# Optimization experiments

Hardware: AMD Instinct MI355X
Metric: run time of the kernel (lower is better)

The kernel has to match this reference:

```python
import jax, jax.numpy as jnp
import numpy as np

EPS = 1e-4

def setup_inputs() -> dict:
    key = jax.random.key(0)
    k1, k2, k3 = jax.random.split(key, 3)
    batch, keysize, dict_size, categories = 4096, 512, 16384, 100
    x = jax.random.normal(k1, (batch, keysize), dtype=jnp.float32)
    keys = jax.random.normal(k2, (dict_size, keysize), dtype=jnp.float32) * 0.1  # TruncatedNormal(0, 0.1) approx
    values = jax.random.uniform(k3, (dict_size, categories), dtype=jnp.float32)
    return {"x": x, "keys": keys, "values": values}


def reference(x, keys, values):
    # sq_distance(keys, x): (dict_size, batch)
    kk = jnp.sum(keys * keys, axis=1)[:, None]          # (D, 1)
    xx = jnp.sum(x * x, axis=1)[None, :]                # (1, B)
    d = kk - 2.0 * jnp.matmul(keys, x.T) + xx           # (D, B)
    kern = 1.0 / (d + EPS)                              # reciprocal kernel
    # transpose -> (B, D), matmul values (D, C) -> (B, C)
    return jnp.matmul(kern.T, values)
```

## Files before the change

### kernel.cpp

```cpp
#include <hip/hip_runtime.h>
#include <hip/hip_bf16.h>
#include <hip/hip_fp8.h>
#include <cstdint>


#define BSZ   4096
#define DSZ   16384
#define KSZ   512
#define CC    100
#define CP    128
#define EPSV  1e-4f

#define BM     64
#define BD     64
#define DSPLIT 8
#define DCHUNK (DSZ / DSPLIT)
#define NITER  (DCHUNK / BD)
#define KTS    72

typedef short  short8 __attribute__((ext_vector_type(8)));
typedef float  f32x4  __attribute__((ext_vector_type(4)));
typedef long   lng2   __attribute__((ext_vector_type(2)));
typedef unsigned int   u32;
typedef unsigned short u16;
typedef unsigned char  u8;

__device__ __forceinline__ u16 f2bf(float f) {
    union { float f; u32 u; } cv; cv.f = f;
    u32 u = cv.u;
    u += 0x7fffu + ((u >> 16) & 1u);
    return (u16)(u >> 16);
}
__device__ __forceinline__ u32 pack2(float a, float b) {
    return (u32)f2bf(a) | ((u32)f2bf(b) << 16);
}
__device__ __forceinline__ u8 f2fp8(float f) {
    __hip_fp8_e4m3 t(f);
    return *reinterpret_cast<u8*>(&t);
}

__device__ __forceinline__ void gload_lds16(const void* g, void* l) {
    __builtin_amdgcn_global_load_lds(
        (const __attribute__((address_space(1))) u32*)g,
        (__attribute__((address_space(3))) u32*)l, 16, 0, 0);
}


__global__ __launch_bounds__(256)
void convert_xk(const float* __restrict__ x, const float* __restrict__ keys,
                u8* __restrict__ xw, u8* __restrict__ kw,
                float* __restrict__ kk, float* __restrict__ xx)
{
    const int tid = threadIdx.x, wid = tid >> 6, lane = tid & 63;
    const int row = blockIdx.x * 4 + wid;
    const float* src; u8* dst; float* nrm; int r;
    if (row < DSZ) { r = row;       src = keys + (size_t)r * KSZ; dst = kw + (size_t)r * KSZ; nrm = kk + r; }
    else           { r = row - DSZ; src = x    + (size_t)r * KSZ; dst = xw + (size_t)r * KSZ; nrm = xx + r; }

    float4 v0 = *reinterpret_cast<const float4*>(src + lane * 8);
    float4 v1 = *reinterpret_cast<const float4*>(src + lane * 8 + 4);
    float s = v0.x*v0.x + v0.y*v0.y + v0.z*v0.z + v0.w*v0.w
            + v1.x*v1.x + v1.y*v1.y + v1.z*v1.z + v1.w*v1.w;

    unsigned long long pk = 0;
    pk |= (unsigned long long)f2fp8(v0.x);
    pk |= (unsigned long long)f2fp8(v0.y) << 8;
    pk |= (unsigned long long)f2fp8(v0.z) << 16;
    pk |= (unsigned long long)f2fp8(v0.w) << 24;
    pk |= (unsigned long long)f2fp8(v1.x) << 32;
    pk |= (unsigned long long)f2fp8(v1.y) << 40;
    pk |= (unsigned long long)f2fp8(v1.z) << 48;
    pk |= (unsigned long long)f2fp8(v1.w) << 56;

    const int j = lane >> 2, hi_l = lane & 3;
    const int ch = j >> 3, jl = j & 7, jj = jl >> 1, f = jl & 1;
    const int off = ch * 256 + (((jj * 64 + hi_l * 16)) ^ ((r & 7) << 4)) + f * 8;
    *reinterpret_cast<unsigned long long*>(dst + off) = pk;

    s += __shfl_xor(s, 1);  s += __shfl_xor(s, 2);  s += __shfl_xor(s, 4);
    s += __shfl_xor(s, 8);  s += __shfl_xor(s, 16); s += __shfl_xor(s, 32);
    if (lane == 0) *nrm = s;
}

__global__ __launch_bounds__(256)
void convert_v(const float* __restrict__ values, u16* __restrict__ vw)
{
    const int gid = blockIdx.x * 256 + threadIdx.x;
    const int c = gid >> 11;
    const int j = gid & 2047;
    const int dp  = ((j >> 3) << 6) + ((j & 7) << 3);
    const int dsg = ((j >> 3) << 6) + (((j & 7) ^ (c & 7)) << 3);
    uint4 w = make_uint4(0, 0, 0, 0);
    if (c < CC) {
        float f[8];
#pragma unroll
        for (int i = 0; i < 8; ++i) f[i] = values[(size_t)(dsg + i) * CC + c];
        w.x = pack2(f[0], f[1]); w.y = pack2(f[2], f[3]);
        w.z = pack2(f[4], f[5]); w.w = pack2(f[6], f[7]);
    }
    *reinterpret_cast<uint4*>(vw + (size_t)c * DSZ + dp) = w;
}

__global__ __launch_bounds__(512, 4)
void varkeys_fast(const u8* __restrict__ xw, const u8* __restrict__ kw,
                  const u16* __restrict__ vw, const float* __restrict__ kkp,
                  const float* __restrict__ xxp, float* __restrict__ out)
{
    __shared__ __align__(16) u8  ksb0[BD * 256];
    __shared__ __align__(16) u8  ksb1[BD * 256];
    __shared__ __align__(16) u16 kT[BM * KTS];
    __shared__ __align__(16) u16 vT[CP * BD];
    __shared__ float xx_s[BM];

    const int tid  = threadIdx.x;
    const int wid  = tid >> 6;
    const int lane = tid & 63;
    const int lo   = lane & 15;
    const int hi   = lane >> 4;
    const int wm   = wid >> 1;
    const int wn   = wid & 1;

    const int h  = blockIdx.x;
    const int by = h & 7, bx = h >> 3;
    const int bm0   = bx * BM;
    const int dbase = by * DCHUNK;

    if (tid < BM) xx_s[tid] = xxp[bm0 + tid];

    lng2 xq[8];
    {
        const int row = bm0 + wm * 16 + lo;
        const u8* base = xw + (size_t)row * KSZ;
        const int s16 = (row & 7) << 4;
#pragma unroll
        for (int ch = 0; ch < 2; ++ch)
#pragma unroll
            for (int jj = 0; jj < 4; ++jj)
                xq[ch * 4 + jj] = *reinterpret_cast<const lng2*>(
                    base + ch * 256 + ((jj * 64 + hi * 16) ^ s16));
    }

    f32x4 accO[4];
#pragma unroll
    for (int n = 0; n < 4; ++n) accO[n] = f32x4{0.f, 0.f, 0.f, 0.f};

#define IS_KS(BUFP, DK, CCH) { \
        _Pragma("unroll") \
        for (int i = 0; i < 2; ++i) { \
            const int ci = wid * 2 + i; \
            const int flat = ci * 1024 + lane * 16; \
            gload_lds16(kw + (size_t)((DK) + (flat >> 8)) * KSZ + (CCH) * 256 + (flat & 255), \
                        (char*)(BUFP) + ci * 1024); \
        } }

#define IS_VT(D0) { \
        _Pragma("unroll") \
        for (int i = 0; i < 2; ++i) { \
            const int ci = wid * 2 + i; \
            const int flat = ci * 512 + lane * 8; \
            gload_lds16(vw + (size_t)(flat >> 6) * DSZ + (D0) + (flat & 63), \
                        (char*)vT + ci * 1024); \
        } }

    IS_KS(ksb0, dbase, 0)
    asm volatile("s_waitcnt lgkmcnt(0)" ::: "memory");
    __builtin_amdgcn_s_barrier();

    const int swz   = (lo & 7) << 3;
    const int swz16 = (lo & 7) << 4;

#define A16(CH, BUF)                                                                  \
    {                                                                                 \
        _Pragma("unroll")                                                             \
        for (int jj = 0; jj < 4; ++jj) {                                              \
            const int off = (jj * 64 + hi * 16) ^ swz16;                              \
            const u8* p0 = (const u8*)(BUF) + (wn * 32 + lo) * 256 + off;             \
            lng2 b0 = *reinterpret_cast<const lng2*>(p0);                             \
            lng2 b1 = *reinterpret_cast<const lng2*>(p0 + 16 * 256);                  \
            lng2 a0 = xq[(CH) * 4 + jj];                                              \
            accS[0] = __builtin_amdgcn_mfma_f32_16x16x32_fp8_fp8(a0[0], b0[0], accS[0], 0, 0, 0); \
            accS[1] = __builtin_amdgcn_mfma_f32_16x16x32_fp8_fp8(a0[0], b1[0], accS[1], 0, 0, 0); \
            accS[0] = __builtin_amdgcn_mfma_f32_16x16x32_fp8_fp8(a0[1], b0[1], accS[0], 0, 0, 0); \
            accS[1] = __builtin_amdgcn_mfma_f32_16x16x32_fp8_fp8(a0[1], b1[1], accS[1], 0, 0, 0); \
        }                                                                             \
    }

    for (int it = 0; it < NITER; ++it) {
        const int d0 = dbase + it * BD;

        f32x4 accS[2];
#pragma unroll
        for (int n = 0; n < 2; ++n) accS[n] = f32x4{0.f, 0.f, 0.f, 0.f};

        __builtin_amdgcn_s_barrier();
        IS_KS(ksb1, d0, 1)
        IS_VT(d0)
        const float kkf0 = kkp[d0 + wn * 32 + lo];
        const float kkf1 = kkp[d0 + wn * 32 + 16 + lo];
        asm volatile("s_waitcnt vmcnt(6)" ::: "memory");
        __builtin_amdgcn_s_barrier();
        __builtin_amdgcn_sched_barrier(0);
        A16(0, ksb0)

        __builtin_amdgcn_s_barrier();
        if (it < NITER - 1) {
            IS_KS(ksb0, d0 + BD, 0)
            asm volatile("s_waitcnt vmcnt(6)" ::: "memory");
        } else {
            asm volatile("s_waitcnt vmcnt(0)" ::: "memory");
        }
        __builtin_amdgcn_s_barrier();
        __builtin_amdgcn_sched_barrier(0);
        A16(1, ksb1)

#pragma unroll
        for (int n = 0; n < 2; ++n) {
            const int dl = wn * 32 + n * 16 + lo;
            const float kkv = n ? kkf1 : kkf0;
#pragma unroll
            for (int r = 0; r < 4; ++r) {
                const int rowl = wm * 16 + hi * 4 + r;
                const float dsq = kkv + xx_s[rowl] - 2.f * accS[n][r] + EPSV;
                kT[rowl * KTS + dl] = f2bf(__builtin_amdgcn_rcpf(dsq));
            }
        }
        asm volatile("s_waitcnt vmcnt(2)" ::: "memory");
        asm volatile("s_waitcnt lgkmcnt(0)" ::: "memory");
        __builtin_amdgcn_s_barrier();
        __builtin_amdgcn_sched_barrier(0);

#pragma unroll
        for (int kst = 0; kst < 2; ++kst) {
            const int k0l = kst * 32 + hi * 8;
            const int k0v = k0l ^ swz;
            short8 a0 = *reinterpret_cast<const short8*>(&kT[(wm * 16 + lo) * KTS + k0l]);
#pragma unroll
            for (int nh = 0; nh < 2; ++nh) {
                short8 b0 = *reinterpret_cast<const short8*>(&vT[(wn * 64 + nh * 32 + lo) * BD + k0v]);
                short8 b1 = *reinterpret_cast<const short8*>(&vT[(wn * 64 + nh * 32 + 16 + lo) * BD + k0v]);
                accO[nh * 2 + 0] = __builtin_amdgcn_mfma_f32_16x16x32_bf16(a0, b0, accO[nh * 2 + 0], 0, 0, 0);
                accO[nh * 2 + 1] = __builtin_amdgcn_mfma_f32_16x16x32_bf16(a0, b1, accO[nh * 2 + 1], 0, 0, 0);
            }
        }
    }

#pragma unroll
    for (int n = 0; n < 4; ++n) {
        const int c = wn * 64 + n * 16 + lo;
        if (c < CC) {
#pragma unroll
            for (int r = 0; r < 4; ++r) {
                const int b_ = bm0 + wm * 16 + hi * 4 + r;
                atomicAdd(&out[(size_t)b_ * CC + c], accO[n][r]);
            }
        }
    }
#undef IS_KS
#undef IS_VT
#undef A16
}


#define FBM 128
#define XS_STRIDE 72
#define KS_STRIDE 72
#define KT_STRIDE 72
#define VL_STRIDE 106
#define FKC 64
#define FNKC (KSZ / FKC)
#define FDSPLIT 8
#define FDCHUNK (DSZ / FDSPLIT)
#define FNITER  (FDCHUNK / BD)

__global__ __launch_bounds__(256)
void varkeys_pre(const float* __restrict__ x, const float* __restrict__ keys,
                 float* __restrict__ kk, float* __restrict__ xx)
{
    const int tid  = threadIdx.x;
    const int wid  = tid >> 6;
    const int lane = tid & 63;
    const int lo   = lane & 15;
    const int sub  = lane >> 4;
    const int row  = blockIdx.x * 16 + wid * 4 + sub;
    const float* src = (row < DSZ) ? keys + (size_t)row * KSZ
                                   : x + (size_t)(row - DSZ) * KSZ;
    float s = 0.f;
#pragma unroll
    for (int j = 0; j < 8; ++j) {
        float4 v = *reinterpret_cast<const float4*>(src + j * 64 + lo * 4);
        s += v.x * v.x + v.y * v.y + v.z * v.z + v.w * v.w;
    }
    s += __shfl_xor(s, 1); s += __shfl_xor(s, 2);
    s += __shfl_xor(s, 4); s += __shfl_xor(s, 8);
    if (lo == 0) {
        if (row < DSZ) kk[row] = s;
        else           xx[row - DSZ] = s;
    }
}

__global__ __launch_bounds__(256, 2)
void varkeys_main(const float* __restrict__ x, const float* __restrict__ keys,
                  const float* __restrict__ values, float* __restrict__ out,
                  const float* __restrict__ kk_ws, const float* __restrict__ xx_ws,
                  int use_ws)
{
    __shared__ __align__(16) u16 xs[FBM * XS_STRIDE];
    __shared__ __align__(16) u16 ks[BD * KS_STRIDE];
    __shared__ __align__(16) u16 kTf[FBM * KT_STRIDE];
    __shared__ __align__(16) u16 vls[BD * VL_STRIDE];
    __shared__ float kk_s[FDCHUNK];
    __shared__ float xx_s[FBM];

    const int tid  = threadIdx.x;
    const int wid  = tid >> 6;
    const int lane = tid & 63;
    const int lo   = lane & 15;
    const int hi   = lane >> 4;
    const int wm   = wid >> 1;
    const int wn   = wid & 1;
    const int bm0   = blockIdx.x * FBM;
    const int dbase = blockIdx.y * FDCHUNK;

    if (use_ws) {
        for (int i = tid; i < FDCHUNK; i += 256) kk_s[i] = kk_ws[dbase + i];
        if (tid < FBM) xx_s[tid] = xx_ws[bm0 + tid];
    } else {
        for (int rbase = wid * 4; rbase < FDCHUNK + FBM; rbase += 16) {
            const int row = rbase + hi;
            const float* src = (row < FDCHUNK)
                ? keys + (size_t)(dbase + row) * KSZ
                : x + (size_t)(bm0 + row - FDCHUNK) * KSZ;
            float s = 0.f;
#pragma unroll
            for (int j = 0; j < 8; ++j) {
                float4 v = *reinterpret_cast<const float4*>(src + j * 64 + lo * 4);
                s += v.x * v.x + v.y * v.y + v.z * v.z + v.w * v.w;
            }
            s += __shfl_xor(s, 1); s += __shfl_xor(s, 2);
            s += __shfl_xor(s, 4); s += __shfl_xor(s, 8);
            if (lo == 0) {
                if (row < FDCHUNK) kk_s[row] = s;
                else               xx_s[row - FDCHUNK] = s;
            }
        }
    }
    __syncthreads();

    f32x4 accO[4][4];
#pragma unroll
    for (int m = 0; m < 4; ++m)
#pragma unroll
        for (int n = 0; n < 4; ++n) accO[m][n] = f32x4{0.f, 0.f, 0.f, 0.f};

    for (int it = 0; it < FNITER; ++it) {
        const int d0 = dbase + it * BD;

        f32x4 accS[4][2];
#pragma unroll
        for (int m = 0; m < 4; ++m)
#pragma unroll
            for (int n = 0; n < 2; ++n) accS[m][n] = f32x4{0.f, 0.f, 0.f, 0.f};

        for (int kc = 0; kc < FNKC; ++kc) {
            __syncthreads();
#pragma unroll
            for (int j = 0; j < 8; ++j) {
                const int idx = tid + j * 256;
                const int row = idx >> 4, c4 = idx & 15;
                float4 v = *reinterpret_cast<const float4*>(
                    x + (size_t)(bm0 + row) * KSZ + kc * FKC + c4 * 4);
                u32* dst = reinterpret_cast<u32*>(&xs[row * XS_STRIDE + c4 * 4]);
                dst[0] = pack2(v.x, v.y); dst[1] = pack2(v.z, v.w);
            }
#pragma unroll
            for (int j = 0; j < 4; ++j) {
                const int idx = tid + j * 256;
                const int row = idx >> 4, c4 = idx & 15;
                float4 v = *reinterpret_cast<const float4*>(
                    keys + (size_t)(d0 + row) * KSZ + kc * FKC + c4 * 4);
                u32* dst = reinterpret_cast<u32*>(&ks[row * KS_STRIDE + c4 * 4]);
                dst[0] = pack2(v.x, v.y); dst[1] = pack2(v.z, v.w);
            }
            __syncthreads();
#pragma unroll
            for (int kst = 0; kst < 2; ++kst) {
                const int k0 = kst * 32 + hi * 8;
                short8 a[4], b[2];
#pragma unroll
                for (int m = 0; m < 4; ++m)
                    a[m] = *reinterpret_cast<const short8*>(
                        &xs[(wm * 64 + m * 16 + lo) * XS_STRIDE + k0]);
#pragma unroll
                for (int n = 0; n < 2; ++n)
                    b[n] = *reinterpret_cast<const short8*>(
                        &ks[(wn * 32 + n * 16 + lo) * KS_STRIDE + k0]);
#pragma unroll
                for (int m = 0; m < 4; ++m)
#pragma unroll
                    for (int n = 0; n < 2; ++n)
                        accS[m][n] = __builtin_amdgcn_mfma_f32_16x16x32_bf16(
                            a[m], b[n], accS[m][n], 0, 0, 0);
            }
        }

#pragma unroll
        for (int m = 0; m < 4; ++m)
#pragma unroll
            for (int n = 0; n < 2; ++n) {
                const int dl = wn * 32 + n * 16 + lo;
                const float kkv = kk_s[it * BD + dl];
#pragma unroll
                for (int r = 0; r < 4; ++r) {
                    const int bl = wm * 64 + m * 16 + hi * 4 + r;
                    const float dsq = kkv + xx_s[bl] - 2.f * accS[m][n][r] + EPSV;
                    kTf[bl * KT_STRIDE + dl] = f2bf(__builtin_amdgcn_rcpf(dsq));
                }
            }

#pragma unroll
        for (int j = 0; j < 7; ++j) {
            const int idx = tid + j * 256;
            if (idx < 1600) {
                const int row = idx / 25, c4 = idx % 25;
                float4 v = *reinterpret_cast<const float4*>(
                    values + (size_t)(d0 + row) * CC + c4 * 4);
                u32* dst = reinterpret_cast<u32*>(&vls[row * VL_STRIDE + c4 * 4]);
                dst[0] = pack2(v.x, v.y); dst[1] = pack2(v.z, v.w);
            }
        }
        __syncthreads();

#pragma unroll
        for (int ks2 = 0; ks2 < 2; ++ks2) {
            const int k0 = ks2 * 32 + hi * 8;
            short8 a[4], b[4];
#pragma unroll
            for (int m = 0; m < 4; ++m)
                a[m] = *reinterpret_cast<const short8*>(
                    &kTf[(wm * 64 + m * 16 + lo) * KT_STRIDE + k0]);
#pragma unroll
            for (int n = 0; n < 4; ++n) {
                const int c = wn * 64 + n * 16 + lo;
                short8 t = {0, 0, 0, 0, 0, 0, 0, 0};
                if (c < CC) {
#pragma unroll
                    for (int i = 0; i < 8; ++i)
                        t[i] = (short)vls[(k0 + i) * VL_STRIDE + c];
                }
                b[n] = t;
            }
#pragma unroll
            for (int m = 0; m < 4; ++m)
#pragma unroll
                for (int n = 0; n < 4; ++n)
                    accO[m][n] = __builtin_amdgcn_mfma_f32_16x16x32_bf16(
                        a[m], b[n], accO[m][n], 0, 0, 0);
        }
    }

#pragma unroll
    for (int m = 0; m < 4; ++m)
#pragma unroll
        for (int n = 0; n < 4; ++n) {
            const int c = wn * 64 + n * 16 + lo;
            if (c < CC) {
#pragma unroll
                for (int r = 0; r < 4; ++r) {
                    const int b_ = bm0 + wm * 64 + m * 16 + hi * 4 + r;
                    atomicAdd(&out[(size_t)b_ * CC + c], accO[m][n][r]);
                }
            }
        }
}

extern "C" void kernel_launch(void* const* d_in, const int* in_sizes, int n_in,
                              void* d_out, int out_size, void* d_ws, size_t ws_size,
                              hipStream_t stream) {
    const float* x      = (const float*)d_in[0];
    const float* keys   = (const float*)d_in[1];
    const float* values = (const float*)d_in[2];
    float* out = (float*)d_out;

    hipMemsetAsync(d_out, 0, (size_t)out_size * sizeof(float), stream);

    const size_t off_xw = 0;
    const size_t off_kw = off_xw + (size_t)BSZ * KSZ;
    const size_t off_vw = off_kw + (size_t)DSZ * KSZ;
    const size_t off_kk = off_vw + (size_t)CP * DSZ * 2;
    const size_t off_xx = off_kk + (size_t)DSZ * 4;
    const size_t need   = off_xx + (size_t)BSZ * 4;

    if (ws_size >= need) {
        u8*  xw = (u8*)((char*)d_ws + off_xw);
        u8*  kw = (u8*)((char*)d_ws + off_kw);
        u16* vw = (u16*)((char*)d_ws + off_vw);
        float* kk = (float*)((char*)d_ws + off_kk);
        float* xx = (float*)((char*)d_ws + off_xx);
        convert_xk<<<dim3((DSZ + BSZ) / 4), dim3(256), 0, stream>>>(x, keys, xw, kw, kk, xx);
        convert_v<<<dim3((CP * DSZ / 8) / 256), dim3(256), 0, stream>>>(values, vw);
        varkeys_fast<<<dim3(DSPLIT * (BSZ / BM)), dim3(512), 0, stream>>>(xw, kw, vw, kk, xx, out);
    } else {
        const size_t ws_need = (size_t)(DSZ + BSZ) * sizeof(float);
        const int use_ws = (ws_size >= ws_need) ? 1 : 0;
        float* kk = (float*)d_ws;
        float* xx = kk + DSZ;
        if (use_ws) {
            varkeys_pre<<<dim3((DSZ + BSZ) / 16), dim3(256), 0, stream>>>(x, keys, kk, xx);
        }
        varkeys_main<<<dim3(BSZ / FBM, FDSPLIT), dim3(256), 0, stream>>>(
            x, keys, values, out, kk, xx, use_ws);
    }
}
```

Baseline: 114.6 us.

## Merge conversion kernels, keep x norms in registers, skip padded-column MFMAs

The two preprocessing kernels become one launch whose blocks branch by index into either the x/keys fp8 conversion or the values bf16 transpose, removing one launch and its gap. The main kernel drops the shared xx buffer and loads each row's norm, with epsilon folded in, straight into registers. It also removes the initial lgkmcnt wait. It skips the last 16-column MFMA and its LDS load for the second wave column, since those columns are padding beyond 100 categories. The savings are small per-iteration costs, and the register norm load adds a few global loads per thread.

```diff
diff --git a/kernel.cpp b/kernel.cpp
--- a/kernel.cpp
+++ b/kernel.cpp
@@ -45,60 +45,62 @@
         (__attribute__((address_space(3))) u32*)l, 16, 0, 0);
 }
 
+#define XK_BLOCKS ((DSZ + BSZ) / 4)
+#define V_BLOCKS  ((CP * DSZ / 8) / 256)
 
 __global__ __launch_bounds__(256)
-void convert_xk(const float* __restrict__ x, const float* __restrict__ keys,
-                u8* __restrict__ xw, u8* __restrict__ kw,
-                float* __restrict__ kk, float* __restrict__ xx)
+void convert_all(const float* __restrict__ x, const float* __restrict__ keys,
+                 const float* __restrict__ values,
+                 u8* __restrict__ xw, u8* __restrict__ kw, u16* __restrict__ vw,
+                 float* __restrict__ kk, float* __restrict__ xx)
 {
-    const int tid = threadIdx.x, wid = tid >> 6, lane = tid & 63;
-    const int row = blockIdx.x * 4 + wid;
-    const float* src; u8* dst; float* nrm; int r;
-    if (row < DSZ) { r = row;       src = keys + (size_t)r * KSZ; dst = kw + (size_t)r * KSZ; nrm = kk + r; }
-    else           { r = row - DSZ; src = x    + (size_t)r * KSZ; dst = xw + (size_t)r * KSZ; nrm = xx + r; }
-
-    float4 v0 = *reinterpret_cast<const float4*>(src + lane * 8);
-    float4 v1 = *reinterpret_cast<const float4*>(src + lane * 8 + 4);
-    float s = v0.x*v0.x + v0.y*v0.y + v0.z*v0.z + v0.w*v0.w
-            + v1.x*v1.x + v1.y*v1.y + v1.z*v1.z + v1.w*v1.w;
-
-    unsigned long long pk = 0;
-    pk |= (unsigned long long)f2fp8(v0.x);
-    pk |= (unsigned long long)f2fp8(v0.y) << 8;
-    pk |= (unsigned long long)f2fp8(v0.z) << 16;
-    pk |= (unsigned long long)f2fp8(v0.w) << 24;
-    pk |= (unsigned long long)f2fp8(v1.x) << 32;
-    pk |= (unsigned long long)f2fp8(v1.y) << 40;
-    pk |= (unsigned long long)f2fp8(v1.z) << 48;
-    pk |= (unsigned long long)f2fp8(v1.w) << 56;
-
-    const int j = lane >> 2, hi_l = lane & 3;
-    const int ch = j >> 3, jl = j & 7, jj = jl >> 1, f = jl & 1;
-    const int off = ch * 256 + (((jj * 64 + hi_l * 16)) ^ ((r & 7) << 4)) + f * 8;
-    *reinterpret_cast<unsigned long long*>(dst + off) = pk;
-
-    s += __shfl_xor(s, 1);  s += __shfl_xor(s, 2);  s += __shfl_xor(s, 4);
-    s += __shfl_xor(s, 8);  s += __shfl_xor(s, 16); s += __shfl_xor(s, 32);
-    if (lane == 0) *nrm = s;
-}
-
-__global__ __launch_bounds__(256)
-void convert_v(const float* __restrict__ values, u16* __restrict__ vw)
-{
-    const int gid = blockIdx.x * 256 + threadIdx.x;
-    const int c = gid >> 11;
-    const int j = gid & 2047;
-    const int dp  = ((j >> 3) << 6) + ((j & 7) << 3);
-    const int dsg = ((j >> 3) << 6) + (((j & 7) ^ (c & 7)) << 3);
-    uint4 w = make_uint4(0, 0, 0, 0);
-    if (c < CC) {
-        float f[8];
-#pragma unroll
-        for (int i = 0; i < 8; ++i) f[i] = values[(size_t)(dsg + i) * CC + c];
-        w.x = pack2(f[0], f[1]); w.y = pack2(f[2], f[3]);
-        w.z = pack2(f[4], f[5]); w.w = pack2(f[6], f[7]);
-    }
-    *reinterpret_cast<uint4*>(vw + (size_t)c * DSZ + dp) = w;
+    const int tid = threadIdx.x;
+    if (blockIdx.x < XK_BLOCKS) {
+        const int wid = tid >> 6, lane = tid & 63;
+        const int row = blockIdx.x * 4 + wid;
+        const float* src; u8* dst; float* nrm; int r;
+        if (row < DSZ) { r = row;       src = keys + (size_t)r * KSZ; dst = kw + (size_t)r * KSZ; nrm = kk + r; }
+        else           { r = row - DSZ; src = x    + (size_t)r * KSZ; dst = xw + (size_t)r * KSZ; nrm = xx + r; }
+
+        float4 v0 = *reinterpret_cast<const float4*>(src + lane * 8);
+        float4 v1 = *reinterpret_cast<const float4*>(src + lane * 8 + 4);
+        float s = v0.x*v0.x + v0.y*v0.y + v0.z*v0.z + v0.w*v0.w
+                + v1.x*v1.x + v1.y*v1.y + v1.z*v1.z + v1.w*v1.w;
+
+        unsigned long long pk = 0;
+        pk |= (unsigned long long)f2fp8(v0.x);
+        pk |= (unsigned long long)f2fp8(v0.y) << 8;
+        pk |= (unsigned long long)f2fp8(v0.z) << 16;
+        pk |= (unsigned long long)f2fp8(v0.w) << 24;
+        pk |= (unsigned long long)f2fp8(v1.x) << 32;
+        pk |= (unsigned long long)f2fp8(v1.y) << 40;
+        pk |= (unsigned long long)f2fp8(v1.z) << 48;
+        pk |= (unsigned long long)f2fp8(v1.w) << 56;
+
+        const int j = lane >> 2, hi_l = lane & 3;
+        const int ch = j >> 3, jl = j & 7, jj = jl >> 1, f = jl & 1;
+        const int off = ch * 256 + (((jj * 64 + hi_l * 16)) ^ ((r & 7) << 4)) + f * 8;
+        *reinterpret_cast<unsigned long long*>(dst + off) = pk;
+
+        s += __shfl_xor(s, 1);  s += __shfl_xor(s, 2);  s += __shfl_xor(s, 4);
+        s += __shfl_xor(s, 8);  s += __shfl_xor(s, 16); s += __shfl_xor(s, 32);
+        if (lane == 0) *nrm = s;
+    } else {
+        const int gid = (blockIdx.x - XK_BLOCKS) * 256 + tid;
+        const int c = gid >> 11;
+        const int j = gid & 2047;
+        const int dp  = ((j >> 3) << 6) + ((j & 7) << 3);
+        const int dsg = ((j >> 3) << 6) + (((j & 7) ^ (c & 7)) << 3);
+        uint4 w = make_uint4(0, 0, 0, 0);
+        if (c < CC) {
+            float f[8];
+#pragma unroll
+            for (int i = 0; i < 8; ++i) f[i] = values[(size_t)(dsg + i) * CC + c];
+            w.x = pack2(f[0], f[1]); w.y = pack2(f[2], f[3]);
+            w.z = pack2(f[4], f[5]); w.w = pack2(f[6], f[7]);
+        }
+        *reinterpret_cast<uint4*>(vw + (size_t)c * DSZ + dp) = w;
+    }
 }
 
 __global__ __launch_bounds__(512, 4)
@@ -110,7 +112,6 @@
     __shared__ __align__(16) u8  ksb1[BD * 256];
     __shared__ __align__(16) u16 kT[BM * KTS];
     __shared__ __align__(16) u16 vT[CP * BD];
-    __shared__ float xx_s[BM];
 
     const int tid  = threadIdx.x;
     const int wid  = tid >> 6;
@@ -125,8 +126,6 @@
     const int bm0   = bx * BM;
     const int dbase = by * DCHUNK;
 
-    if (tid < BM) xx_s[tid] = xxp[bm0 + tid];
-
     lng2 xq[8];
     {
         const int row = bm0 + wm * 16 + lo;
@@ -139,6 +138,10 @@
                 xq[ch * 4 + jj] = *reinterpret_cast<const lng2*>(
                     base + ch * 256 + ((jj * 64 + hi * 16) ^ s16));
     }
+    float xr[4];
+#pragma unroll
+    for (int r = 0; r < 4; ++r)
+        xr[r] = xxp[bm0 + wm * 16 + hi * 4 + r] + EPSV;
 
     f32x4 accO[4];
 #pragma unroll
@@ -163,7 +166,6 @@
         } }
 
     IS_KS(ksb0, dbase, 0)
-    asm volatile("s_waitcnt lgkmcnt(0)" ::: "memory");
     __builtin_amdgcn_s_barrier();
 
     const int swz   = (lo & 7) << 3;
@@ -220,7 +222,7 @@
 #pragma unroll
             for (int r = 0; r < 4; ++r) {
                 const int rowl = wm * 16 + hi * 4 + r;
-                const float dsq = kkv + xx_s[rowl] - 2.f * accS[n][r] + EPSV;
+                const float dsq = kkv + xr[r] - 2.f * accS[n][r];
                 kT[rowl * KTS + dl] = f2bf(__builtin_amdgcn_rcpf(dsq));
             }
         }
@@ -237,9 +239,11 @@
 #pragma unroll
             for (int nh = 0; nh < 2; ++nh) {
                 short8 b0 = *reinterpret_cast<const short8*>(&vT[(wn * 64 + nh * 32 + lo) * BD + k0v]);
-                short8 b1 = *reinterpret_cast<const short8*>(&vT[(wn * 64 + nh * 32 + 16 + lo) * BD + k0v]);
                 accO[nh * 2 + 0] = __builtin_amdgcn_mfma_f32_16x16x32_bf16(a0, b0, accO[nh * 2 + 0], 0, 0, 0);
-                accO[nh * 2 + 1] = __builtin_amdgcn_mfma_f32_16x16x32_bf16(a0, b1, accO[nh * 2 + 1], 0, 0, 0);
+                if (wn == 0 || nh == 0) {
+                    short8 b1 = *reinterpret_cast<const short8*>(&vT[(wn * 64 + nh * 32 + 16 + lo) * BD + k0v]);
+                    accO[nh * 2 + 1] = __builtin_amdgcn_mfma_f32_16x16x32_bf16(a0, b1, accO[nh * 2 + 1], 0, 0, 0);
+                }
             }
         }
     }
@@ -496,8 +500,8 @@
         u16* vw = (u16*)((char*)d_ws + off_vw);
         float* kk = (float*)((char*)d_ws + off_kk);
         float* xx = (float*)((char*)d_ws + off_xx);
-        convert_xk<<<dim3((DSZ + BSZ) / 4), dim3(256), 0, stream>>>(x, keys, xw, kw, kk, xx);
-        convert_v<<<dim3((CP * DSZ / 8) / 256), dim3(256), 0, stream>>>(values, vw);
+        convert_all<<<dim3(XK_BLOCKS + V_BLOCKS), dim3(256), 0, stream>>>(
+            x, keys, values, xw, kw, vw, kk, xx);
         varkeys_fast<<<dim3(DSPLIT * (BSZ / BM)), dim3(512), 0, stream>>>(xw, kw, vw, kk, xx, out);
     } else {
         const size_t ws_need = (size_t)(DSZ + BSZ) * sizeof(float);
```

New measurement: 112.2 us. 2.1% less time.
